# Performance work log

Hardware: AMD Instinct MI355X
Metric: run time of the kernel (lower is better)

Reference implementation:

```python
import jax, jax.numpy as jnp
import numpy as np

N_HEADS = 16
HEAD_DIM = 64
HIDDEN = N_HEADS * HEAD_DIM


def setup_inputs() -> dict:
    key = jax.random.key(0)
    ks = jax.random.split(key, 10)
    B, F, T = 2, 2048, 2048
    std = 0.02
    inp = {
        "from_tensor": jax.random.normal(ks[0], (B, F, HIDDEN), dtype=jnp.float32),
        "to_tensor": jax.random.normal(ks[1], (B, T, HIDDEN), dtype=jnp.float32),
        "attention_mask": jax.random.randint(ks[2], (B, F, T), 0, 2, dtype=jnp.int32),
        "Wq": jax.random.normal(ks[3], (HIDDEN, HIDDEN), dtype=jnp.float32) * std,
        "bq": jnp.zeros((HIDDEN,), dtype=jnp.float32),
        "Wk": jax.random.normal(ks[4], (HIDDEN, HIDDEN), dtype=jnp.float32) * std,
        "bk": jnp.zeros((HIDDEN,), dtype=jnp.float32),
        "Wv": jax.random.normal(ks[5], (HIDDEN, HIDDEN), dtype=jnp.float32) * std,
        "bv": jnp.zeros((HIDDEN,), dtype=jnp.float32),
    }
    return inp


def reference(from_tensor, to_tensor, attention_mask, Wq, bq, Wk, bk, Wv, bv):
    B, F, _ = from_tensor.shape
    T = to_tensor.shape[1]
    N, H = N_HEADS, HEAD_DIM

    # QKV projections (no activations: query/key/value act fns are None)
    q = (from_tensor @ Wq + bq).reshape(B, F, N, H)
    k = (to_tensor @ Wk + bk).reshape(B, T, N, H)
    v = (to_tensor @ Wv + bv).reshape(B, T, N, H)

    scores = jnp.einsum('BFNH,BTNH->BNFT', q, k) * (1.0 / np.sqrt(float(H)))
    # additive mask: mask [B,F,T] -> [B,1,F,T]; 0 entries get -10000
    adder = (1.0 - attention_mask.astype(jnp.float32))[:, None, :, :] * -10000.0
    scores = scores + adder
    probs = jax.nn.softmax(scores, axis=-1)  # dropout skipped (inference)

    context = jnp.einsum('BNFT,BTNH->BFNH', probs, v)
    return context.reshape(B, F, N * H)
```

## Files before the change

kernel.cpp:

```cpp
#include <hip/hip_runtime.h>


typedef short v8s __attribute__((ext_vector_type(8)));
typedef float v4f __attribute__((ext_vector_type(4)));
typedef unsigned short u16;
typedef unsigned int   u32;
typedef unsigned long long u64;

constexpr float QSCALE = 0.18033688011112042f;

__device__ __forceinline__ u16 f2bf(float f) {
    u32 u = __builtin_bit_cast(u32, f);
    u += 0x7fffu + ((u >> 16) & 1u);
    return (u16)(u >> 16);
}

__device__ __forceinline__ u32 pack_trunc(float a, float b) {
    u32 ua = __builtin_bit_cast(u32, a);
    u32 ub = __builtin_bit_cast(u32, b);
    return (ua >> 16) | (ub & 0xffff0000u);
}

__device__ __forceinline__ v8s ld8(const u16* p) {
    return *reinterpret_cast<const v8s*>(p);
}

__device__ __forceinline__ void async16(const void* g, void* l) {
    __builtin_amdgcn_global_load_lds(
        (const __attribute__((address_space(1))) u32*)g,
        (__attribute__((address_space(3))) u32*)l, 16, 0, 0);
}

__global__ __launch_bounds__(256) void prep(
    const float* __restrict__ from, const float* __restrict__ to,
    u16* __restrict__ Xf, u16* __restrict__ Xt,
    const float* __restrict__ Wq, const float* __restrict__ Wk, const float* __restrict__ Wv,
    u16* __restrict__ Wqt, u16* __restrict__ Wkt, u16* __restrict__ Wvt,
    const int* __restrict__ mask, u64* __restrict__ words) {
    __shared__ float tile[32][33];
    const int bid = blockIdx.x, tid = threadIdx.x;
    if (bid < 8192) {
        int i = bid * 256 + tid;
        const float4* s;
        ushort4* d;
        int j;
        if (i < 1048576) { s = (const float4*)from; d = (ushort4*)Xf; j = i; }
        else             { s = (const float4*)to;   d = (ushort4*)Xt; j = i - 1048576; }
        float4 v = s[j];
        ushort4 o;
        o.x = f2bf(v.x); o.y = f2bf(v.y); o.z = f2bf(v.z); o.w = f2bf(v.w);
        d[j] = o;
    } else if (bid < 11264) {
        const int r = bid - 8192;
        const int zz = r >> 10, rem = r & 1023;
        const float* W = zz == 0 ? Wq : (zz == 1 ? Wk : Wv);
        u16* Wt = zz == 0 ? Wqt : (zz == 1 ? Wkt : Wvt);
        const int tx = tid & 31, ty = tid >> 5;
        const int n0 = (rem & 31) * 32, k0 = (rem >> 5) * 32;
        for (int i = 0; i < 4; i++)
            tile[ty + i * 8][tx] = W[(size_t)(k0 + ty + i * 8) * 1024 + n0 + tx];
        __syncthreads();
        for (int i = 0; i < 4; i++)
            Wt[(size_t)(n0 + ty + i * 8) * 1024 + k0 + tx] = f2bf(tile[tx][ty + i * 8]);
    } else {
        int g = (bid - 11264) * 256 + tid;
        int w = g >> 6, lane = g & 63;
        int v = mask[(size_t)w * 64 + lane];
        u64 bits = __ballot(v != 0);
        if (lane == 0) words[w] = bits;
    }
}

__global__ __launch_bounds__(256) void gemm_qkv(
    const u16* __restrict__ Xf, const u16* __restrict__ Xt,
    const u16* __restrict__ Wqt, const u16* __restrict__ Wkt, const u16* __restrict__ Wvt,
    const float* __restrict__ bq, const float* __restrict__ bk, const float* __restrict__ bv,
    u16* __restrict__ Qb, u16* __restrict__ Kb, u16* __restrict__ Vtb) {
    const int z = blockIdx.z;
    const u16* A      = z == 0 ? Xf : Xt;
    const u16* Bt     = z == 0 ? Wqt : (z == 1 ? Wkt : Wvt);
    const float* bias = z == 0 ? bq : (z == 1 ? bk : bv);
    u16* C            = z == 0 ? Qb : (z == 1 ? Kb : Vtb);
    const int mode    = (z == 2);
    const float sc    = (z == 0) ? QSCALE : 1.0f;

    __shared__ u16 As[2][128][32];
    __shared__ u16 Bs[2][128][32];
    const uint4* Ag = reinterpret_cast<const uint4*>(A);
    const uint4* Bg = reinterpret_cast<const uint4*>(Bt);

    const int tid = threadIdx.x;
    const int lane = tid & 63, wave = tid >> 6;
    const int quad = lane >> 4, l16 = lane & 15;
    const int wm = wave >> 1, wn = wave & 1;
    const int m0 = blockIdx.x * 128, n0 = blockIdx.y * 128;

    const int cg  = (lane & 3) ^ ((lane >> 3) & 3);
    const int sw8 = (quad ^ ((l16 >> 1) & 3)) * 8;

    const int gi0 = wave * 4;
    const uint4 *ap0, *ap1, *ap2, *ap3, *bp0, *bp1, *bp2, *bp3;
    {
        const int rl = lane >> 2;
        const int rb0 = ((gi0 + 0) & 7) * 16 + rl, kh0 = (gi0 + 0) >> 3;
        const int rb1 = ((gi0 + 1) & 7) * 16 + rl, kh1 = (gi0 + 1) >> 3;
        const int rb2 = ((gi0 + 2) & 7) * 16 + rl, kh2 = (gi0 + 2) >> 3;
        const int rb3 = ((gi0 + 3) & 7) * 16 + rl, kh3 = (gi0 + 3) >> 3;
        ap0 = Ag + (size_t)(m0 + rb0) * 128 + kh0 * 4 + cg;
        ap1 = Ag + (size_t)(m0 + rb1) * 128 + kh1 * 4 + cg;
        ap2 = Ag + (size_t)(m0 + rb2) * 128 + kh2 * 4 + cg;
        ap3 = Ag + (size_t)(m0 + rb3) * 128 + kh3 * 4 + cg;
        bp0 = Bg + (size_t)(n0 + rb0) * 128 + kh0 * 4 + cg;
        bp1 = Bg + (size_t)(n0 + rb1) * 128 + kh1 * 4 + cg;
        bp2 = Bg + (size_t)(n0 + rb2) * 128 + kh2 * 4 + cg;
        bp3 = Bg + (size_t)(n0 + rb3) * 128 + kh3 * 4 + cg;
    }
    u16* Asl = (u16*)As + gi0 * 512;
    u16* Bsl = (u16*)Bs + gi0 * 512;

    v4f acc[4][4];
    for (int i = 0; i < 4; i++)
        for (int j = 0; j < 4; j++) acc[i][j] = (v4f)0.0f;

    for (int k0 = 0; k0 < 16; k0++) {
        __syncthreads();
        async16(ap0, Asl);        ap0 += 8;
        async16(ap1, Asl + 512);  ap1 += 8;
        async16(ap2, Asl + 1024); ap2 += 8;
        async16(ap3, Asl + 1536); ap3 += 8;
        async16(bp0, Bsl);        bp0 += 8;
        async16(bp1, Bsl + 512);  bp1 += 8;
        async16(bp2, Bsl + 1024); bp2 += 8;
        async16(bp3, Bsl + 1536); bp3 += 8;
        __syncthreads();

        #pragma unroll
        for (int kk = 0; kk < 2; kk++) {
            v8s af[4], bf[4];
            #pragma unroll
            for (int mt = 0; mt < 4; mt++) af[mt] = ld8(&As[kk][wm * 64 + mt * 16 + l16][sw8]);
            #pragma unroll
            for (int nt = 0; nt < 4; nt++) bf[nt] = ld8(&Bs[kk][wn * 64 + nt * 16 + l16][sw8]);
            #pragma unroll
            for (int mt = 0; mt < 4; mt++)
                #pragma unroll
                for (int nt = 0; nt < 4; nt++)
                    acc[mt][nt] = __builtin_amdgcn_mfma_f32_16x16x32_bf16(af[mt], bf[nt], acc[mt][nt], 0, 0, 0);
        }
    }

    #pragma unroll
    for (int nt = 0; nt < 4; nt++) {
        const int col = n0 + wn * 64 + nt * 16 + l16;
        const float bvv = bias[col];
        #pragma unroll
        for (int mt = 0; mt < 4; mt++) {
            const int mbase = m0 + wm * 64 + mt * 16 + quad * 4;
            if (mode == 0) {
                for (int r = 0; r < 4; r++)
                    C[(size_t)(mbase + r) * 1024 + col] = f2bf((acc[mt][nt][r] + bvv) * sc);
            } else {
                const int b = mbase >> 11, t = mbase & 2047;
                const int head = col >> 6, h = col & 63;
                ushort4 pk;
                pk.x = f2bf(acc[mt][nt][0] + bvv);
                pk.y = f2bf(acc[mt][nt][1] + bvv);
                pk.z = f2bf(acc[mt][nt][2] + bvv);
                pk.w = f2bf(acc[mt][nt][3] + bvv);
                *reinterpret_cast<ushort4*>(&C[(size_t)((b * 16 + head) * 64 + h) * 2048 + t]) = pk;
            }
        }
    }
}

__global__ __launch_bounds__(512, 4) void attn_fused(
    const u16* __restrict__ Qb, const u16* __restrict__ Kb,
    const u16* __restrict__ Vtb, const u64* __restrict__ mw,
    float* __restrict__ out) {
    __shared__ u16 Ks[2][2][64][32];
    __shared__ u16 Vs[2][2][64][32];
    __shared__ u32 Ps[8 * 1152];

    const int tid = threadIdx.x;
    const int lane = tid & 63, wave = tid >> 6;
    const int quad = lane >> 4, l16 = lane & 15;
    const int fwave = wave & 3, tw = wave >> 2;
    const int b = blockIdx.x >> 4, head = blockIdx.x & 15;
    const int f0 = blockIdx.y * 128;

    const uint4* Kg = reinterpret_cast<const uint4*>(Kb);
    const uint4* Vg = reinterpret_cast<const uint4*>(Vtb);
    const size_t vbase4 = (size_t)(b * 16 + head) * 64 * 256;

    const int cg  = (lane & 3) ^ ((lane >> 3) & 3);
    const int sw8 = (quad ^ ((l16 >> 1) & 3)) * 8;

    v8s qf[2][2];
    #pragma unroll
    for (int kk = 0; kk < 2; kk++)
        #pragma unroll
        for (int qh = 0; qh < 2; qh++)
            qf[kk][qh] = ld8(Qb + ((size_t)(b * 2048 + f0 + fwave * 32 + qh * 16 + l16) * 16 + head) * 64
                                + kk * 32 + quad * 8);

    v8s ones;
    #pragma unroll
    for (int i = 0; i < 8; i++) ones[i] = (short)0x3F80;

    const uint4 *sp0, *sp1, *sp2, *sp3;
    u16 *sd;
    size_t sinc;
    {
        const int rl = lane >> 2;
        if (wave < 4) {
            const int g0 = wave * 4;
            sd = (u16*)Ks + g0 * 512;
            sinc = 8192;
            #define KPTR(g) (Kg + ((size_t)(b * 2048 + ((g) >> 3) * 1024 + ((g) & 3) * 16 + rl) * 16 + head) * 8 \
                                + (((g) >> 2) & 1) * 4 + cg)
            sp0 = KPTR(g0); sp1 = KPTR(g0 + 1); sp2 = KPTR(g0 + 2); sp3 = KPTR(g0 + 3);
            #undef KPTR
        } else {
            const int g0 = (wave - 4) * 4;
            sd = (u16*)Vs + g0 * 512;
            sinc = 8;
            #define VPTR(g) (Vg + vbase4 + (size_t)(((g) & 3) * 16 + rl) * 256 + ((g) >> 3) * 128 \
                                + (((g) >> 2) & 1) * 4 + cg)
            sp0 = VPTR(g0); sp1 = VPTR(g0 + 1); sp2 = VPTR(g0 + 2); sp3 = VPTR(g0 + 3);
            #undef VPTR
        }
    }

    v4f accO[2][4], accL[2];
    #pragma unroll
    for (int qh = 0; qh < 2; qh++) {
        accL[qh] = (v4f)0.0f;
        for (int ht = 0; ht < 4; ht++) accO[qh][ht] = (v4f)0.0f;
    }

    u32* myPs = Ps + wave * 1152;
    const u64* mrow = mw + (size_t)(b * 2048 + f0 + fwave * 32 + l16) * 32 + tw * 16;

    for (int it = 0; it < 16; it++) {
        __syncthreads();
        async16(sp0, sd);        sp0 += sinc;
        async16(sp1, sd + 512);  sp1 += sinc;
        async16(sp2, sd + 1024); sp2 += sinc;
        async16(sp3, sd + 1536); sp3 += sinc;
        __syncthreads();

        v4f s[2][4];
        #pragma unroll
        for (int qh = 0; qh < 2; qh++)
            for (int mt = 0; mt < 4; mt++) s[qh][mt] = (v4f)0.0f;
        #pragma unroll
        for (int kk = 0; kk < 2; kk++) {
            v8s kf[4];
            #pragma unroll
            for (int mt = 0; mt < 4; mt++) kf[mt] = ld8(&Ks[tw][kk][mt * 16 + l16][sw8]);
            #pragma unroll
            for (int qh = 0; qh < 2; qh++)
                #pragma unroll
                for (int mt = 0; mt < 4; mt++)
                    s[qh][mt] = __builtin_amdgcn_mfma_f32_16x16x32_bf16(kf[mt], qf[kk][qh], s[qh][mt], 0, 0, 0);
        }

        u32 pk[2][8];
        #pragma unroll
        for (int qh = 0; qh < 2; qh++) {
            const u64 w = mrow[qh * 512 + it];
            const u32 lo = (u32)(w >> (quad * 4));
            const u32 hi = (u32)(w >> (quad * 4 + 32));
            #pragma unroll
            for (int mt = 0; mt < 4; mt++) {
                const u32 bits = ((mt & 2) ? hi : lo) >> ((mt & 1) * 16);
                float p[4];
                #pragma unroll
                for (int r = 0; r < 4; r++) {
                    const float e = __builtin_amdgcn_exp2f(s[qh][mt][r]);
                    p[r] = ((bits >> r) & 1u) ? e : 0.0f;
                }
                pk[qh][mt * 2]     = pack_trunc(p[0], p[1]);
                pk[qh][mt * 2 + 1] = pack_trunc(p[2], p[3]);
            }
        }

        #pragma unroll
        for (int qh = 0; qh < 2; qh++) {
            const int row = qh * 16 + l16;
            #pragma unroll
            for (int mt = 0; mt < 4; mt++)
                *reinterpret_cast<uint2*>(&myPs[row * 36 + mt * 8 + quad * 2]) =
                    make_uint2(pk[qh][mt * 2], pk[qh][mt * 2 + 1]);
        }

        #pragma unroll
        for (int kk = 0; kk < 2; kk++) {
            v8s vf[4];
            #pragma unroll
            for (int ht = 0; ht < 4; ht++) vf[ht] = ld8(&Vs[tw][kk][ht * 16 + l16][sw8]);
            #pragma unroll
            for (int qh = 0; qh < 2; qh++) {
                const v8s pf = *reinterpret_cast<const v8s*>(
                    &myPs[(qh * 16 + l16) * 36 + kk * 16 + quad * 4]);
                #pragma unroll
                for (int ht = 0; ht < 4; ht++)
                    accO[qh][ht] = __builtin_amdgcn_mfma_f32_16x16x32_bf16(vf[ht], pf, accO[qh][ht], 0, 0, 0);
                accL[qh] = __builtin_amdgcn_mfma_f32_16x16x32_bf16(ones, pf, accL[qh], 0, 0, 0);
            }
        }
    }

    __syncthreads();
    float* fb = (float*)Ps;
    if (tw == 1) {
        float* wdst = fb + fwave * 2304 + lane * 36;
        #pragma unroll
        for (int qh = 0; qh < 2; qh++)
            #pragma unroll
            for (int ht = 0; ht < 4; ht++)
                *reinterpret_cast<v4f*>(wdst + (qh * 4 + ht) * 4) = accO[qh][ht];
        wdst[32] = accL[0][0];
        wdst[33] = accL[1][0];
    }
    __syncthreads();
    if (tw == 0) {
        const float* rsrc = fb + fwave * 2304 + lane * 36;
        float inv[2];
        #pragma unroll
        for (int qh = 0; qh < 2; qh++)
            inv[qh] = 1.0f / (accL[qh][0] + rsrc[32 + qh]);
        #pragma unroll
        for (int qh = 0; qh < 2; qh++) {
            const size_t ro = (size_t)(b * 2048 + f0 + fwave * 32 + qh * 16 + l16) * 1024 + head * 64;
            #pragma unroll
            for (int ht = 0; ht < 4; ht++) {
                const v4f p = *reinterpret_cast<const v4f*>(rsrc + (qh * 4 + ht) * 4);
                float4 o;
                o.x = (accO[qh][ht][0] + p[0]) * inv[qh];
                o.y = (accO[qh][ht][1] + p[1]) * inv[qh];
                o.z = (accO[qh][ht][2] + p[2]) * inv[qh];
                o.w = (accO[qh][ht][3] + p[3]) * inv[qh];
                *reinterpret_cast<float4*>(&out[ro + ht * 16 + quad * 4]) = o;
            }
        }
    }
}

extern "C" void kernel_launch(void* const* d_in, const int* in_sizes, int n_in,
                              void* d_out, int out_size, void* d_ws, size_t ws_size,
                              hipStream_t stream) {
    const float* from = (const float*)d_in[0];
    const float* to   = (const float*)d_in[1];
    const int*   mask = (const int*)d_in[2];
    const float* Wq = (const float*)d_in[3];
    const float* bq = (const float*)d_in[4];
    const float* Wk = (const float*)d_in[5];
    const float* bk = (const float*)d_in[6];
    const float* Wv = (const float*)d_in[7];
    const float* bv = (const float*)d_in[8];
    float* out = (float*)d_out;

    u16* Xf  = (u16*)d_ws;
    u16* Xt  = Xf  + 4194304;
    u16* Wqt = Xt  + 4194304;
    u16* Wkt = Wqt + 1048576;
    u16* Wvt = Wkt + 1048576;
    u16* Qb  = Wvt + 1048576;
    u16* Kb  = Qb  + 4194304;
    u16* Vtb = Kb  + 4194304;
    u64* mwords = (u64*)(Vtb + 4194304);

    prep<<<44032, 256, 0, stream>>>(from, to, Xf, Xt, Wq, Wk, Wv, Wqt, Wkt, Wvt, mask, mwords);

    gemm_qkv<<<dim3(32, 8, 3), 256, 0, stream>>>(Xf, Xt, Wqt, Wkt, Wvt, bq, bk, bv, Qb, Kb, Vtb);

    attn_fused<<<dim3(32, 16), 512, 0, stream>>>(Qb, Kb, Vtb, mwords, out);
}
```

Baseline: 226.5 us.

## Load K/V fragments directly from global memory, drop shared staging and barriers

Removes the shared-memory staging of K and V tiles along with the two block-wide barriers per iteration. Each wave now loads its K and V MFMA fragments straight from global memory, relying on L1/L2 for reuse across waves. The mask is also folded into the score accumulator's initial value (-15000 for masked entries), so the per-element select after exp2 goes away. The cost is redundant global loads, since the four f-waves sharing a tw each fetch the same K/V, and the masking is now approximate, with masked probabilities only near zero rather than exactly zero.

```diff
diff --git a/kernel.cpp b/kernel.cpp
--- a/kernel.cpp
+++ b/kernel.cpp
@@ -177,8 +177,6 @@
     const u16* __restrict__ Qb, const u16* __restrict__ Kb,
     const u16* __restrict__ Vtb, const u64* __restrict__ mw,
     float* __restrict__ out) {
-    __shared__ u16 Ks[2][2][64][32];
-    __shared__ u16 Vs[2][2][64][32];
     __shared__ u32 Ps[8 * 1152];
 
     const int tid = threadIdx.x;
@@ -187,13 +185,7 @@
     const int fwave = wave & 3, tw = wave >> 2;
     const int b = blockIdx.x >> 4, head = blockIdx.x & 15;
     const int f0 = blockIdx.y * 128;
-
-    const uint4* Kg = reinterpret_cast<const uint4*>(Kb);
-    const uint4* Vg = reinterpret_cast<const uint4*>(Vtb);
-    const size_t vbase4 = (size_t)(b * 16 + head) * 64 * 256;
-
-    const int cg  = (lane & 3) ^ ((lane >> 3) & 3);
-    const int sw8 = (quad ^ ((l16 >> 1) & 3)) * 8;
+    const int tbase = tw * 1024;
 
     v8s qf[2][2];
     #pragma unroll
@@ -207,29 +199,8 @@
     #pragma unroll
     for (int i = 0; i < 8; i++) ones[i] = (short)0x3F80;
 
-    const uint4 *sp0, *sp1, *sp2, *sp3;
-    u16 *sd;
-    size_t sinc;
-    {
-        const int rl = lane >> 2;
-        if (wave < 4) {
-            const int g0 = wave * 4;
-            sd = (u16*)Ks + g0 * 512;
-            sinc = 8192;
-            #define KPTR(g) (Kg + ((size_t)(b * 2048 + ((g) >> 3) * 1024 + ((g) & 3) * 16 + rl) * 16 + head) * 8 \
-                                + (((g) >> 2) & 1) * 4 + cg)
-            sp0 = KPTR(g0); sp1 = KPTR(g0 + 1); sp2 = KPTR(g0 + 2); sp3 = KPTR(g0 + 3);
-            #undef KPTR
-        } else {
-            const int g0 = (wave - 4) * 4;
-            sd = (u16*)Vs + g0 * 512;
-            sinc = 8;
-            #define VPTR(g) (Vg + vbase4 + (size_t)(((g) & 3) * 16 + rl) * 256 + ((g) >> 3) * 128 \
-                                + (((g) >> 2) & 1) * 4 + cg)
-            sp0 = VPTR(g0); sp1 = VPTR(g0 + 1); sp2 = VPTR(g0 + 2); sp3 = VPTR(g0 + 3);
-            #undef VPTR
-        }
-    }
+    const u16* kbase = Kb + ((size_t)(b * 2048 + tbase + l16) * 16 + head) * 64 + quad * 8;
+    const u16* vbase = Vtb + (size_t)(b * 16 + head) * 131072 + (size_t)l16 * 2048 + tbase + quad * 8;
 
     v4f accO[2][4], accL[2];
     #pragma unroll
@@ -242,22 +213,27 @@
     const u64* mrow = mw + (size_t)(b * 2048 + f0 + fwave * 32 + l16) * 32 + tw * 16;
 
     for (int it = 0; it < 16; it++) {
-        __syncthreads();
-        async16(sp0, sd);        sp0 += sinc;
-        async16(sp1, sd + 512);  sp1 += sinc;
-        async16(sp2, sd + 1024); sp2 += sinc;
-        async16(sp3, sd + 1536); sp3 += sinc;
-        __syncthreads();
-
         v4f s[2][4];
         #pragma unroll
-        for (int qh = 0; qh < 2; qh++)
-            for (int mt = 0; mt < 4; mt++) s[qh][mt] = (v4f)0.0f;
+        for (int qh = 0; qh < 2; qh++) {
+            const u64 w = mrow[qh * 512 + it];
+            const u32 lo = (u32)(w >> (quad * 4));
+            const u32 hi = (u32)(w >> (quad * 4 + 32));
+            #pragma unroll
+            for (int mt = 0; mt < 4; mt++) {
+                const u32 bits = ((mt & 2) ? hi : lo) >> ((mt & 1) * 16);
+                #pragma unroll
+                for (int r = 0; r < 4; r++)
+                    s[qh][mt][r] = ((bits >> r) & 1u) ? 0.0f : -15000.0f;
+            }
+        }
+
         #pragma unroll
         for (int kk = 0; kk < 2; kk++) {
             v8s kf[4];
             #pragma unroll
-            for (int mt = 0; mt < 4; mt++) kf[mt] = ld8(&Ks[tw][kk][mt * 16 + l16][sw8]);
+            for (int mt = 0; mt < 4; mt++)
+                kf[mt] = ld8(kbase + (size_t)it * 65536 + mt * 16384 + kk * 32);
             #pragma unroll
             for (int qh = 0; qh < 2; qh++)
                 #pragma unroll
@@ -265,47 +241,36 @@
                     s[qh][mt] = __builtin_amdgcn_mfma_f32_16x16x32_bf16(kf[mt], qf[kk][qh], s[qh][mt], 0, 0, 0);
         }
 
-        u32 pk[2][8];
-        #pragma unroll
-        for (int qh = 0; qh < 2; qh++) {
-            const u64 w = mrow[qh * 512 + it];
-            const u32 lo = (u32)(w >> (quad * 4));
-            const u32 hi = (u32)(w >> (quad * 4 + 32));
-            #pragma unroll
-            for (int mt = 0; mt < 4; mt++) {
-                const u32 bits = ((mt & 2) ? hi : lo) >> ((mt & 1) * 16);
-                float p[4];
-                #pragma unroll
-                for (int r = 0; r < 4; r++) {
-                    const float e = __builtin_amdgcn_exp2f(s[qh][mt][r]);
-                    p[r] = ((bits >> r) & 1u) ? e : 0.0f;
-                }
-                pk[qh][mt * 2]     = pack_trunc(p[0], p[1]);
-                pk[qh][mt * 2 + 1] = pack_trunc(p[2], p[3]);
-            }
-        }
+        v8s vf[2][4];
+        #pragma unroll
+        for (int kk = 0; kk < 2; kk++)
+            #pragma unroll
+            for (int ht = 0; ht < 4; ht++)
+                vf[kk][ht] = ld8(vbase + it * 64 + ht * 32768 + kk * 32);
 
         #pragma unroll
         for (int qh = 0; qh < 2; qh++) {
             const int row = qh * 16 + l16;
             #pragma unroll
-            for (int mt = 0; mt < 4; mt++)
+            for (int mt = 0; mt < 4; mt++) {
+                const float p0 = __builtin_amdgcn_exp2f(s[qh][mt][0]);
+                const float p1 = __builtin_amdgcn_exp2f(s[qh][mt][1]);
+                const float p2 = __builtin_amdgcn_exp2f(s[qh][mt][2]);
+                const float p3 = __builtin_amdgcn_exp2f(s[qh][mt][3]);
                 *reinterpret_cast<uint2*>(&myPs[row * 36 + mt * 8 + quad * 2]) =
-                    make_uint2(pk[qh][mt * 2], pk[qh][mt * 2 + 1]);
+                    make_uint2(pack_trunc(p0, p1), pack_trunc(p2, p3));
+            }
         }
 
         #pragma unroll
         for (int kk = 0; kk < 2; kk++) {
-            v8s vf[4];
-            #pragma unroll
-            for (int ht = 0; ht < 4; ht++) vf[ht] = ld8(&Vs[tw][kk][ht * 16 + l16][sw8]);
             #pragma unroll
             for (int qh = 0; qh < 2; qh++) {
                 const v8s pf = *reinterpret_cast<const v8s*>(
                     &myPs[(qh * 16 + l16) * 36 + kk * 16 + quad * 4]);
                 #pragma unroll
                 for (int ht = 0; ht < 4; ht++)
-                    accO[qh][ht] = __builtin_amdgcn_mfma_f32_16x16x32_bf16(vf[ht], pf, accO[qh][ht], 0, 0, 0);
+                    accO[qh][ht] = __builtin_amdgcn_mfma_f32_16x16x32_bf16(vf[kk][ht], pf, accO[qh][ht], 0, 0, 0);
                 accL[qh] = __builtin_amdgcn_mfma_f32_16x16x32_bf16(ones, pf, accL[qh], 0, 0, 0);
             }
         }
```

Result: slower. 305.1 us (+34.7%).

## Fold mask into score init, halve P staging buffer, raise occupancy target

Applied to the files above, without the earlier changes.

The attention kernel now sets the score accumulator to 0 or -15000 from the mask bits before the QK MFMA, so the per-element select after exp2 is gone. P is staged in LDS one 16-row half at a time, which halves the per-wave scratch, and the final reduction reuses the whole shared buffer. Launch bounds move from 4 to 6 blocks per CU, and the V fragments for both k-steps are loaded before the exp stage. P is now packed with round-to-nearest bf16 conversion instead of truncation. The risks are register spills under the tighter launch bound, and the -15000 bias relies on masked scores staying far below zero after the scale.

```diff
diff --git a/kernel.cpp b/kernel.cpp
--- a/kernel.cpp
+++ b/kernel.cpp
@@ -1,4 +1,5 @@
 #include <hip/hip_runtime.h>
+#include <hip/hip_bf16.h>
 
 
 typedef short v8s __attribute__((ext_vector_type(8)));
@@ -15,10 +16,11 @@
     return (u16)(u >> 16);
 }
 
-__device__ __forceinline__ u32 pack_trunc(float a, float b) {
-    u32 ua = __builtin_bit_cast(u32, a);
-    u32 ub = __builtin_bit_cast(u32, b);
-    return (ua >> 16) | (ub & 0xffff0000u);
+__device__ __forceinline__ u32 pack2(float a, float b) {
+    __hip_bfloat162 h = __float22bfloat162_rn(make_float2(a, b));
+    u32 r;
+    __builtin_memcpy(&r, &h, 4);
+    return r;
 }
 
 __device__ __forceinline__ v8s ld8(const u16* p) {
@@ -173,13 +175,14 @@
     }
 }
 
-__global__ __launch_bounds__(512, 4) void attn_fused(
+__global__ __launch_bounds__(512, 6) void attn_fused(
     const u16* __restrict__ Qb, const u16* __restrict__ Kb,
     const u16* __restrict__ Vtb, const u64* __restrict__ mw,
     float* __restrict__ out) {
-    __shared__ u16 Ks[2][2][64][32];
-    __shared__ u16 Vs[2][2][64][32];
-    __shared__ u32 Ps[8 * 1152];
+    __shared__ __align__(16) char smem[51200];
+    u16* Ks = (u16*)smem;
+    u16* Vs = (u16*)(smem + 16384);
+    u32* Ps = (u32*)(smem + 32768);
 
     const int tid = threadIdx.x;
     const int lane = tid & 63, wave = tid >> 6;
@@ -214,7 +217,7 @@
         const int rl = lane >> 2;
         if (wave < 4) {
             const int g0 = wave * 4;
-            sd = (u16*)Ks + g0 * 512;
+            sd = Ks + g0 * 512;
             sinc = 8192;
             #define KPTR(g) (Kg + ((size_t)(b * 2048 + ((g) >> 3) * 1024 + ((g) & 3) * 16 + rl) * 16 + head) * 8 \
                                 + (((g) >> 2) & 1) * 4 + cg)
@@ -222,7 +225,7 @@
             #undef KPTR
         } else {
             const int g0 = (wave - 4) * 4;
-            sd = (u16*)Vs + g0 * 512;
+            sd = Vs + g0 * 512;
             sinc = 8;
             #define VPTR(g) (Vg + vbase4 + (size_t)(((g) & 3) * 16 + rl) * 256 + ((g) >> 3) * 128 \
                                 + (((g) >> 2) & 1) * 4 + cg)
@@ -238,7 +241,7 @@
         for (int ht = 0; ht < 4; ht++) accO[qh][ht] = (v4f)0.0f;
     }
 
-    u32* myPs = Ps + wave * 1152;
+    u32* myPs = Ps + wave * 576;
     const u64* mrow = mw + (size_t)(b * 2048 + f0 + fwave * 32 + l16) * 32 + tw * 16;
 
     for (int it = 0; it < 16; it++) {
@@ -251,13 +254,25 @@
 
         v4f s[2][4];
         #pragma unroll
-        for (int qh = 0; qh < 2; qh++)
-            for (int mt = 0; mt < 4; mt++) s[qh][mt] = (v4f)0.0f;
+        for (int qh = 0; qh < 2; qh++) {
+            const u64 w = mrow[qh * 512 + it];
+            const u32 lo = (u32)(w >> (quad * 4));
+            const u32 hi = (u32)(w >> (quad * 4 + 32));
+            #pragma unroll
+            for (int mt = 0; mt < 4; mt++) {
+                const u32 bits = ((mt & 2) ? hi : lo) >> ((mt & 1) * 16);
+                #pragma unroll
+                for (int r = 0; r < 4; r++)
+                    s[qh][mt][r] = ((bits >> r) & 1u) ? 0.0f : -15000.0f;
+            }
+        }
+
         #pragma unroll
         for (int kk = 0; kk < 2; kk++) {
             v8s kf[4];
             #pragma unroll
-            for (int mt = 0; mt < 4; mt++) kf[mt] = ld8(&Ks[tw][kk][mt * 16 + l16][sw8]);
+            for (int mt = 0; mt < 4; mt++)
+                kf[mt] = ld8(&Ks[(((tw * 2 + kk) * 64) + mt * 16 + l16) * 32 + sw8]);
             #pragma unroll
             for (int qh = 0; qh < 2; qh++)
                 #pragma unroll
@@ -265,54 +280,38 @@
                     s[qh][mt] = __builtin_amdgcn_mfma_f32_16x16x32_bf16(kf[mt], qf[kk][qh], s[qh][mt], 0, 0, 0);
         }
 
-        u32 pk[2][8];
+        v8s vf[2][4];
+        #pragma unroll
+        for (int kk = 0; kk < 2; kk++)
+            #pragma unroll
+            for (int ht = 0; ht < 4; ht++)
+                vf[kk][ht] = ld8(&Vs[(((tw * 2 + kk) * 64) + ht * 16 + l16) * 32 + sw8]);
+
         #pragma unroll
         for (int qh = 0; qh < 2; qh++) {
-            const u64 w = mrow[qh * 512 + it];
-            const u32 lo = (u32)(w >> (quad * 4));
-            const u32 hi = (u32)(w >> (quad * 4 + 32));
             #pragma unroll
             for (int mt = 0; mt < 4; mt++) {
-                const u32 bits = ((mt & 2) ? hi : lo) >> ((mt & 1) * 16);
-                float p[4];
-                #pragma unroll
-                for (int r = 0; r < 4; r++) {
-                    const float e = __builtin_amdgcn_exp2f(s[qh][mt][r]);
-                    p[r] = ((bits >> r) & 1u) ? e : 0.0f;
-                }
-                pk[qh][mt * 2]     = pack_trunc(p[0], p[1]);
-                pk[qh][mt * 2 + 1] = pack_trunc(p[2], p[3]);
-            }
-        }
-
-        #pragma unroll
-        for (int qh = 0; qh < 2; qh++) {
-            const int row = qh * 16 + l16;
-            #pragma unroll
-            for (int mt = 0; mt < 4; mt++)
-                *reinterpret_cast<uint2*>(&myPs[row * 36 + mt * 8 + quad * 2]) =
-                    make_uint2(pk[qh][mt * 2], pk[qh][mt * 2 + 1]);
-        }
-
-        #pragma unroll
-        for (int kk = 0; kk < 2; kk++) {
-            v8s vf[4];
-            #pragma unroll
-            for (int ht = 0; ht < 4; ht++) vf[ht] = ld8(&Vs[tw][kk][ht * 16 + l16][sw8]);
-            #pragma unroll
-            for (int qh = 0; qh < 2; qh++) {
+                const float p0 = __builtin_amdgcn_exp2f(s[qh][mt][0]);
+                const float p1 = __builtin_amdgcn_exp2f(s[qh][mt][1]);
+                const float p2 = __builtin_amdgcn_exp2f(s[qh][mt][2]);
+                const float p3 = __builtin_amdgcn_exp2f(s[qh][mt][3]);
+                *reinterpret_cast<uint2*>(&myPs[l16 * 36 + mt * 8 + quad * 2]) =
+                    make_uint2(pack2(p0, p1), pack2(p2, p3));
+            }
+            #pragma unroll
+            for (int kk = 0; kk < 2; kk++) {
                 const v8s pf = *reinterpret_cast<const v8s*>(
-                    &myPs[(qh * 16 + l16) * 36 + kk * 16 + quad * 4]);
+                    &myPs[l16 * 36 + kk * 16 + quad * 4]);
                 #pragma unroll
                 for (int ht = 0; ht < 4; ht++)
-                    accO[qh][ht] = __builtin_amdgcn_mfma_f32_16x16x32_bf16(vf[ht], pf, accO[qh][ht], 0, 0, 0);
+                    accO[qh][ht] = __builtin_amdgcn_mfma_f32_16x16x32_bf16(vf[kk][ht], pf, accO[qh][ht], 0, 0, 0);
                 accL[qh] = __builtin_amdgcn_mfma_f32_16x16x32_bf16(ones, pf, accL[qh], 0, 0, 0);
             }
         }
     }
 
     __syncthreads();
-    float* fb = (float*)Ps;
+    float* fb = (float*)smem;
     if (tw == 1) {
         float* wdst = fb + fwave * 2304 + lane * 36;
         #pragma unroll
```

Result: slower. 527.2 us (+132.8%).
